# Performance work log

Hardware: AMD Instinct MI355X
Metric: run time of the kernel (lower is better)

Reference implementation:

```python
import jax, jax.numpy as jnp
import numpy as np

PHI = 1.618033988749895  # golden ratio
LUT_SIZE = 4096
TWO_PI = 2.0 * float(np.pi)
_grid = np.arange(LUT_SIZE, dtype=np.float32) * (TWO_PI / LUT_SIZE)
SIN_TABLE = jnp.asarray(np.sin(_grid).astype(np.float32))
COS_TABLE = jnp.asarray(np.cos(_grid).astype(np.float32))


def lut_sin_cos(theta):
    """4096-entry sin/cos lookup table over [0, 2pi) with linear interpolation."""
    pos = theta * (LUT_SIZE / TWO_PI)
    i0 = jnp.floor(pos)
    frac = (pos - i0).astype(theta.dtype)
    idx0 = jnp.mod(i0.astype(jnp.int32), LUT_SIZE)
    idx1 = jnp.mod(idx0 + 1, LUT_SIZE)
    sin_v = SIN_TABLE[idx0] * (1.0 - frac) + SIN_TABLE[idx1] * frac
    cos_v = COS_TABLE[idx0] * (1.0 - frac) + COS_TABLE[idx1] * frac
    return sin_v, cos_v


def _forward(input_ids, emb, w_query, b_query, w_key, b_key, w_ctx, W_res, B_res, w_pr, w_pi, w_out):
    B, S = input_ids.shape
    D = emb.shape[1] // 2
    H, dh = w_query.shape
    e = emb[input_ids]                               # [B,S,2D]
    w_emb, b_emb = e[..., :D], e[..., D:]
    t_arr = jnp.arange(S, dtype=jnp.float32)

    # --- sequential euler-transform recurrence (the only truly serial part) ---
    def step(carry, xs):
        h_r, h_i = carry
        w_t, b_t, t = xs                             # [B,D],[B,D],scalar
        wl = 1.0 + jnp.abs(w_t)
        tp = t * PHI
        th_r = h_r / wl + b_t + tp
        th_i = h_i / wl + b_t + tp
        sr, cr = lut_sin_cos(th_r)
        si, ci = lut_sin_cos(th_i)
        nr = cr * ci - sr * si
        ni = cr * si + sr * ci
        return (nr, ni), nr + ni

    init = (jnp.zeros((B, D), dtype=emb.dtype), jnp.zeros((B, D), dtype=emb.dtype))
    xs = (jnp.swapaxes(w_emb, 0, 1), jnp.swapaxes(b_emb, 0, 1), t_arr)
    _, states = jax.lax.scan(step, init, xs)         # [S,B,D]
    states = jnp.swapaxes(states, 0, 1)              # [B,S,D] == cached_states

    # --- multi-head LUT sin/cos attention over strictly-previous cached states ---
    xp = states.reshape(B, S, H, dh)                 # per-head patches
    t_phi = t_arr * PHI                              # [S]
    th_q = xp / (1.0 + jnp.abs(w_query)) + b_query + t_phi[None, :, None, None]
    sq, cq = lut_sin_cos(th_q)
    q = jnp.concatenate([cq, sq], axis=-1)           # [B,S,H,2dh]
    th_k = xp / (1.0 + jnp.abs(w_key)) + b_key
    sk, ck = lut_sin_cos(th_k)
    k = jnp.concatenate([ck, sk], axis=-1)           # [B,S,H,2dh]
    scale = float(np.sqrt(2.0 * dh))
    scores = jnp.einsum('bthd,bshd->bhts', q, k) / scale
    mask = jnp.tril(jnp.ones((S, S), dtype=bool), k=-1)   # keys strictly before query
    scores = jnp.where(mask[None, None], scores, -1e30)
    weights = jax.nn.softmax(scores, axis=-1)
    context = jnp.einsum('bhts,bsd->btd', weights, states)   # heads summed
    has_ctx = (t_arr > 0).astype(states.dtype)[None, :, None]  # t=0 has no cache
    x = states + has_ctx * (context @ w_ctx.T)

    # --- resonant layer over num_neurons ---
    wl_res = 1.0 + jnp.abs(W_res)                    # [N,D]
    theta = x[:, :, None, :] / wl_res + B_res + t_phi[None, :, None, None]  # [B,S,N,D]
    s_t, c_t = lut_sin_cos(theta)
    cos_sum = c_t.sum(-1)                            # [B,S,N]
    sin_sum = s_t.sum(-1)
    x = x + jax.nn.silu(cos_sum @ w_pr.T + sin_sum @ w_pi.T)

    return x @ w_out.T                               # [B,S,V]


def setup_inputs() -> dict:
    key = jax.random.key(0)
    ks = jax.random.split(key, 12)
    B, S, V, D, H, N = 8, 512, 32000, 64, 4, 128
    dh = D // H
    return {
        'input_ids': jax.random.randint(ks[0], (B, S), 0, V),
        'emb': jax.random.normal(ks[1], (V, 2 * D), dtype=jnp.float32) * 0.02,
        'w_query': jax.random.normal(ks[2], (H, dh), dtype=jnp.float32) * 0.02,
        'b_query': jnp.zeros((H, dh), dtype=jnp.float32),
        'w_key': jax.random.normal(ks[3], (H, dh), dtype=jnp.float32) * 0.02,
        'b_key': jnp.zeros((H, dh), dtype=jnp.float32),
        'w_ctx': jax.random.normal(ks[4], (D, D), dtype=jnp.float32) * 0.02,
        'W_res': jax.random.normal(ks[5], (N, D), dtype=jnp.float32) * 0.02,
        'B_res': jnp.zeros((N, D), dtype=jnp.float32),
        'w_pr': jax.random.normal(ks[6], (D, N), dtype=jnp.float32) * 0.02,
        'w_pi': jax.random.normal(ks[7], (D, N), dtype=jnp.float32) * 0.02,
        'w_out': jax.random.normal(ks[8], (V, D), dtype=jnp.float32) * 0.02,
    }


def reference(input_ids, emb, w_query, b_query, w_key, b_key, w_ctx, W_res, B_res, w_pr, w_pi, w_out):
    return _forward(input_ids, emb, w_query, b_query, w_key, b_key, w_ctx, W_res, B_res, w_pr, w_pi, w_out)
```

## Files before the change

### kernel.cpp

```cpp
#include <hip/hip_runtime.h>
#include <hip/hip_bf16.h>
#include <math.h>

#define PHI_F     1.618033988749895f
#define LUT_N     4096
#define LUT_INV   651.8986469044033f
#define LUT_STEP  0.0015339807878856412f

#define B_  8
#define S_  512
#define D_  64
#define H_  4
#define DH_ 16
#define N_  128
#define V_  32000
#define R_  (B_ * S_)

typedef __attribute__((ext_vector_type(8))) short short8_t;
typedef __attribute__((ext_vector_type(4))) float f32x4;

__device__ __forceinline__ void lut2(const float2* __restrict__ sc,
                                     float th, float& s, float& c) {
    float pos = th * LUT_INV;
    float f0  = floorf(pos);
    float fr  = pos - f0;
    int   i0  = ((int)f0) & (LUT_N - 1);
    int   i1  = (i0 + 1) & (LUT_N - 1);
    float2 p0 = sc[i0];
    float2 p1 = sc[i1];
    float om  = 1.0f - fr;
    s = p0.x * om + p1.x * fr;
    c = p0.y * om + p1.y * fr;
}

__global__ void k_tables(float2* __restrict__ scT) {
    int i = blockIdx.x * blockDim.x + threadIdx.x;
    if (i < LUT_N) {
        float g = (float)i * LUT_STEP;
        scT[i] = make_float2((float)sin((double)g), (float)cos((double)g));
    }
}

__global__ __launch_bounds__(256) void k_fused0(
        const int* __restrict__ ids, const float* __restrict__ emb,
        const float* __restrict__ Wres, const float* __restrict__ Bres,
        const float* __restrict__ wpr, const float* __restrict__ wpi,
        const float* __restrict__ wout, const float2* __restrict__ scT,
        float* __restrict__ states, __hip_bfloat16* __restrict__ wb,
        float2* __restrict__ ibres, float2* __restrict__ wpT) {
    int blk = blockIdx.x;
    int tid = threadIdx.x;
    if (blk >= 8) {
        if (blk < 2008) {
            int i = (blk - 8) * 256 + tid;
            float4 v = ((const float4*)wout)[i];
            union { __hip_bfloat16 h[4]; short4 s4; } u;
            u.h[0] = __float2bfloat16(v.x);
            u.h[1] = __float2bfloat16(v.y);
            u.h[2] = __float2bfloat16(v.z);
            u.h[3] = __float2bfloat16(v.w);
            *(short4*)(&wb[4 * (size_t)i]) = u.s4;
        } else {
            int idx = (blk - 2008) * 256 + tid;
            ibres[idx] = make_float2(1.0f / (1.0f + fabsf(Wres[idx])), Bres[idx]);
            int nn = idx >> 6, d = idx & 63;
            wpT[idx] = make_float2(wpr[d * N_ + nn], wpi[d * N_ + nn]);
        }
        return;
    }
    __shared__ float2 sc[LUT_N];
    __shared__ int idsh[S_];
    for (int i = tid; i < LUT_N; i += 256) sc[i] = scT[i];
    for (int i = tid; i < S_; i += 256) idsh[i] = ids[blk * S_ + i];
    __syncthreads();
    if (tid >= 64) return;
    int d = tid, b = blk;
    float cw[8], cb[8], nw[8], nb[8];
#pragma unroll
    for (int j = 0; j < 8; ++j) {
        int id = idsh[j];
        cw[j] = emb[(size_t)id * 128 + d];
        cb[j] = emb[(size_t)id * 128 + 64 + d];
    }
    float* outp = states + (size_t)b * S_ * D_ + d;
    float hr = 0.0f, hi = 0.0f;
    for (int tc = 0; tc < S_; tc += 8) {
#pragma unroll
        for (int jj = 0; jj < 8; ++jj) {
            int id = idsh[(tc + 8 + jj) & (S_ - 1)];
            nw[jj] = emb[(size_t)id * 128 + d];
            nb[jj] = emb[(size_t)id * 128 + 64 + d];
        }
#pragma unroll
        for (int jj = 0; jj < 8; ++jj) {
            int   t   = tc + jj;
            float wl  = 1.0f + fabsf(cw[jj]);
            float btv = cb[jj];
            float tp  = (float)t * PHI_F;
            float thr = hr / wl + btv + tp;
            float thi = hi / wl + btv + tp;
            float sr, cr, si, ci;
            lut2(sc, thr, sr, cr);
            lut2(sc, thi, si, ci);
            float nr = cr * ci - sr * si;
            float ni = cr * si + sr * ci;
            hr = nr; hi = ni;
            outp[t * D_] = nr + ni;
        }
#pragma unroll
        for (int jj = 0; jj < 8; ++jj) { cw[jj] = nw[jj]; cb[jj] = nb[jj]; }
    }
}

__global__ __launch_bounds__(256) void k_qk(const float* __restrict__ states,
                                            const float* __restrict__ wq,
                                            const float* __restrict__ bq,
                                            const float* __restrict__ wk,
                                            const float* __restrict__ bk,
                                            const float2* __restrict__ scT,
                                            float* __restrict__ q,
                                            float* __restrict__ kT) {
    __shared__ float2 sc[LUT_N];
    for (int i = threadIdx.x; i < LUT_N; i += 256) sc[i] = scT[i];
    __syncthreads();
    {
        int idx = blockIdx.x * 256 + threadIdx.x;
        int j  = idx & (DH_ - 1);
        int h  = (idx >> 4) & (H_ - 1);
        int bt = idx >> 6;
        int t  = bt & (S_ - 1);
        int b  = bt >> 9;
        float xp = states[idx];
        float tp = (float)t * PHI_F;
        int   hj = h * DH_ + j;
        float thq = xp / (1.0f + fabsf(wq[hj])) + bq[hj] + tp;
        float thk = xp / (1.0f + fabsf(wk[hj])) + bk[hj];
        float sq, cq, sk, ck;
        lut2(sc, thq, sq, cq);
        lut2(sc, thk, sk, ck);
        int base = bt * (H_ * 2 * DH_) + h * (2 * DH_) + j;
        q[base] = cq; q[base + DH_] = sq;
        size_t kb = ((size_t)(b * H_ + h) * 32 + j) * S_ + t;
        kT[kb] = ck; kT[kb + 16 * S_] = sk;
    }
}

#define TB_ 4
__global__ __launch_bounds__(256) void k_attn(const float* __restrict__ states,
                                              const float* __restrict__ q,
                                              const float* __restrict__ kT,
                                              const float* __restrict__ wctx,
                                              float* __restrict__ x) {
    __shared__ float ql[H_][TB_][2 * DH_];
    __shared__ float wlds[H_][TB_][S_];
    __shared__ float cpart[4][TB_][D_];
    __shared__ float ctx[TB_][D_];
    int blk = blockIdx.x;
    int b = blk >> 7, tile = blk & 127;
    int t0 = tile * TB_;
    int tid = threadIdx.x;
    int h = tid >> 6, l = tid & 63;
    if (l < 2 * DH_) {
#pragma unroll
        for (int tt = 0; tt < TB_; ++tt)
            ql[h][tt][l] = q[((b << 9) + t0 + tt) * 128 + h * 32 + l];
    }
    __syncthreads();

    const float* kTb = kT + (size_t)(b * H_ + h) * 32 * S_;
    float sc[8][TB_];
    float m[TB_];
#pragma unroll
    for (int tt = 0; tt < TB_; ++tt) m[tt] = -INFINITY;
#pragma unroll
    for (int jj = 0; jj < 8; ++jj) {
        int s = l + jj * 64;
        float a0 = 0.f, a1 = 0.f, a2 = 0.f, a3 = 0.f;
        if (s < t0 + TB_ - 1) {
#pragma unroll
            for (int c = 0; c < 32; ++c) {
                float kv = kTb[c * S_ + s];
                a0 = fmaf(kv, ql[h][0][c], a0);
                a1 = fmaf(kv, ql[h][1][c], a1);
                a2 = fmaf(kv, ql[h][2][c], a2);
                a3 = fmaf(kv, ql[h][3][c], a3);
            }
        }
        const float scale = 0.1767766952966369f;
        float v0 = (s < t0 + 0) ? a0 * scale : -INFINITY;
        float v1 = (s < t0 + 1) ? a1 * scale : -INFINITY;
        float v2 = (s < t0 + 2) ? a2 * scale : -INFINITY;
        float v3 = (s < t0 + 3) ? a3 * scale : -INFINITY;
        sc[jj][0] = v0; m[0] = fmaxf(m[0], v0);
        sc[jj][1] = v1; m[1] = fmaxf(m[1], v1);
        sc[jj][2] = v2; m[2] = fmaxf(m[2], v2);
        sc[jj][3] = v3; m[3] = fmaxf(m[3], v3);
    }
#pragma unroll
    for (int tt = 0; tt < TB_; ++tt)
        for (int o = 32; o; o >>= 1) m[tt] = fmaxf(m[tt], __shfl_xor(m[tt], o));
    float sum[TB_] = {0.f, 0.f, 0.f, 0.f};
#pragma unroll
    for (int jj = 0; jj < 8; ++jj)
#pragma unroll
        for (int tt = 0; tt < TB_; ++tt) {
            float e = __expf(sc[jj][tt] - m[tt]);
            sc[jj][tt] = e; sum[tt] += e;
        }
#pragma unroll
    for (int tt = 0; tt < TB_; ++tt)
        for (int o = 32; o; o >>= 1) sum[tt] += __shfl_xor(sum[tt], o);
#pragma unroll
    for (int tt = 0; tt < TB_; ++tt) {
        float inv = 1.0f / sum[tt];
#pragma unroll
        for (int jj = 0; jj < 8; ++jj)
            wlds[h][tt][l + jj * 64] = sc[jj][tt] * inv;
    }
    __syncthreads();
    {
        int p = tid >> 6, d = tid & 63;
        float ac[TB_] = {0.f, 0.f, 0.f, 0.f};
        for (int s = p; s < t0 + TB_ - 1; s += 4) {
            float sv = states[(((size_t)b << 9) + s) * D_ + d];
#pragma unroll
            for (int tt = 0; tt < TB_; ++tt) {
                float w4 = wlds[0][tt][s] + wlds[1][tt][s]
                         + wlds[2][tt][s] + wlds[3][tt][s];
                if (s < t0 + tt) ac[tt] += w4 * sv;
            }
        }
#pragma unroll
        for (int tt = 0; tt < TB_; ++tt) cpart[p][tt][d] = ac[tt];
    }
    __syncthreads();
    {
        int tt = tid >> 6, dd = tid & 63;
        ctx[tt][dd] = cpart[0][tt][dd] + cpart[1][tt][dd]
                    + cpart[2][tt][dd] + cpart[3][tt][dd];
    }
    __syncthreads();
    {
        int tt = tid >> 6, dd = tid & 63;
        int t  = t0 + tt;
        size_t row = ((size_t)b << 9) + t;
        float base = states[row * D_ + dd];
        float val  = base;
        if (t > 0) {
            float y = 0.0f;
            const float* wr = wctx + dd * D_;
            for (int k = 0; k < D_; ++k) y += ctx[tt][k] * wr[k];
            val = base + y;
        }
        x[row * D_ + dd] = val;
    }
}

__global__ __launch_bounds__(256) void k_resid(const float* __restrict__ x,
                                               const float2* __restrict__ ibres,
                                               const float2* __restrict__ wpT,
                                               const float2* __restrict__ scT,
                                               __hip_bfloat16* __restrict__ xb) {
    __shared__ float2 sc[LUT_N];
    __shared__ float xv[D_];
    __shared__ float csum[N_], ssum[N_];
    __shared__ float part[4][D_];
    int tid = threadIdx.x;
    for (int i = tid; i < LUT_N; i += 256) sc[i] = scT[i];
    int n  = tid >> 1;
    int d0 = (tid & 1) * 32;
    float2 ib[32];
#pragma unroll
    for (int dd = 0; dd < 32; ++dd) ib[dd] = ibres[n * D_ + d0 + dd];
    int g = tid >> 6, dl = tid & 63;
    for (int r = 0; r < 8; ++r) {
        int bt = blockIdx.x * 8 + r;
        int t  = bt & (S_ - 1);
        float tp = (float)t * PHI_F;
        __syncthreads();
        if (tid < D_) xv[tid] = x[bt * D_ + tid];
        __syncthreads();
        float cs = 0.0f, ss = 0.0f;
#pragma unroll
        for (int dd = 0; dd < 32; ++dd) {
            float th = fmaf(xv[d0 + dd], ib[dd].x, ib[dd].y) + tp;
            float s, c;
            lut2(sc, th, s, c);
            cs += c; ss += s;
        }
        cs += __shfl_xor(cs, 1);
        ss += __shfl_xor(ss, 1);
        if ((tid & 1) == 0) { csum[n] = cs; ssum[n] = ss; }
        __syncthreads();
        float acc = 0.0f;
#pragma unroll
        for (int nn = 0; nn < 32; ++nn) {
            float2 w = wpT[(g * 32 + nn) * D_ + dl];
            acc = fmaf(csum[g * 32 + nn], w.x, fmaf(ssum[g * 32 + nn], w.y, acc));
        }
        part[g][dl] = acc;
        __syncthreads();
        if (tid < D_) {
            float pre = part[0][tid] + part[1][tid] + part[2][tid] + part[3][tid];
            float sig = 1.0f / (1.0f + __expf(-pre));
            xb[bt * D_ + tid] = __float2bfloat16(xv[tid] + pre * sig);
        }
    }
}

__global__ __launch_bounds__(256) void k_out(const __hip_bfloat16* __restrict__ xb,
                                             const __hip_bfloat16* __restrict__ wb,
                                             float* __restrict__ out) {
    __shared__ float ot[64][132];
    int tid  = threadIdx.x;
    int wave = tid >> 6, l = tid & 63;
    int wr = wave >> 1, wc = wave & 1;
    int m0 = blockIdx.y * 64 + wr * 32;
    int r  = l & 15;
    int ks = (l >> 4) * 8;
    int kh = l >> 4;

    short8_t a[2][2];
#pragma unroll
    for (int mi = 0; mi < 2; ++mi)
#pragma unroll
        for (int kk = 0; kk < 2; ++kk)
            a[mi][kk] = *reinterpret_cast<const short8_t*>(
                xb + (size_t)(m0 + mi * 16 + r) * 64 + kk * 32 + ks);

    for (int ch = 0; ch < 2; ++ch) {
        int c0 = blockIdx.x * 256 + ch * 128 + wc * 64;
        short8_t b[4][2];
#pragma unroll
        for (int ni = 0; ni < 4; ++ni)
#pragma unroll
            for (int kk = 0; kk < 2; ++kk)
                b[ni][kk] = *reinterpret_cast<const short8_t*>(
                    wb + (size_t)(c0 + ni * 16 + r) * 64 + kk * 32 + ks);

        f32x4 acc[2][4];
#pragma unroll
        for (int mi = 0; mi < 2; ++mi)
#pragma unroll
            for (int ni = 0; ni < 4; ++ni) {
                acc[mi][ni] = (f32x4){0.f, 0.f, 0.f, 0.f};
                acc[mi][ni] = __builtin_amdgcn_mfma_f32_16x16x32_bf16(
                    a[mi][0], b[ni][0], acc[mi][ni], 0, 0, 0);
                acc[mi][ni] = __builtin_amdgcn_mfma_f32_16x16x32_bf16(
                    a[mi][1], b[ni][1], acc[mi][ni], 0, 0, 0);
            }

        if (ch) __syncthreads();
#pragma unroll
        for (int mi = 0; mi < 2; ++mi)
#pragma unroll
            for (int ni = 0; ni < 4; ++ni)
#pragma unroll
                for (int i = 0; i < 4; ++i)
                    ot[wr * 32 + mi * 16 + kh * 4 + i][wc * 64 + ni * 16 + r] = acc[mi][ni][i];
        __syncthreads();

        size_t rbase = blockIdx.y * 64;
        size_t cb    = (size_t)blockIdx.x * 256 + ch * 128;
#pragma unroll
        for (int j = 0; j < 8; ++j) {
            int idx = j * 256 + tid;
            int row = idx >> 5, c4 = idx & 31;
            f32x4 v = *(const f32x4*)&ot[row][c4 * 4];
            __builtin_nontemporal_store(v,
                (f32x4*)&out[(rbase + row) * V_ + cb + c4 * 4]);
        }
    }
}

extern "C" void kernel_launch(void* const* d_in, const int* in_sizes, int n_in,
                              void* d_out, int out_size, void* d_ws, size_t ws_size,
                              hipStream_t stream) {
    const int*   ids  = (const int*)  d_in[0];
    const float* emb  = (const float*)d_in[1];
    const float* wq   = (const float*)d_in[2];
    const float* bq   = (const float*)d_in[3];
    const float* wk   = (const float*)d_in[4];
    const float* bk   = (const float*)d_in[5];
    const float* wctx = (const float*)d_in[6];
    const float* Wres = (const float*)d_in[7];
    const float* Bres = (const float*)d_in[8];
    const float* wpr  = (const float*)d_in[9];
    const float* wpi  = (const float*)d_in[10];
    const float* wout = (const float*)d_in[11];
    float* out = (float*)d_out;

    float* states = (float*)d_ws;
    float* qbuf   = states + R_ * D_;
    float* kTbuf  = qbuf + R_ * 128;
    float* xbuf   = kTbuf + B_ * H_ * 32 * S_;
    __hip_bfloat16* wb = (__hip_bfloat16*)(xbuf + R_ * D_);
    __hip_bfloat16* xb = wb + (size_t)V_ * D_;
    float2* scT   = (float2*)(xb + R_ * D_);
    float2* ibres = scT + LUT_N;
    float2* wpT   = ibres + N_ * D_;

    k_tables<<<16, 256, 0, stream>>>(scT);
    k_fused0<<<2040, 256, 0, stream>>>(ids, emb, Wres, Bres, wpr, wpi, wout, scT,
                                       states, wb, ibres, wpT);
    k_qk    <<<1024, 256, 0, stream>>>(states, wq, bq, wk, bk, scT, qbuf, kTbuf);
    k_attn  <<<1024, 256, 0, stream>>>(states, qbuf, kTbuf, wctx, xbuf);
    k_resid <<<R_ / 8, 256, 0, stream>>>(xbuf, ibres, wpT, scT, xb);
    k_out   <<<dim3(V_ / 256, R_ / 64), 256, 0, stream>>>(xb, wb, out);
}
```

Before: 326.0 us.

## Use paired float4 LUT in recurrence, drop LDS tables in qk, batch resid loads

```diff
diff --git a/kernel.cpp b/kernel.cpp
--- a/kernel.cpp
+++ b/kernel.cpp
@@ -33,11 +33,15 @@
     c = p0.y * om + p1.y * fr;
 }
 
-__global__ void k_tables(float2* __restrict__ scT) {
+__global__ void k_tables(float2* __restrict__ scT2, float4* __restrict__ scT4) {
     int i = blockIdx.x * blockDim.x + threadIdx.x;
     if (i < LUT_N) {
         float g = (float)i * LUT_STEP;
-        scT[i] = make_float2((float)sin((double)g), (float)cos((double)g));
+        float s = (float)sin((double)g);
+        float c = (float)cos((double)g);
+        scT2[i] = make_float2(s, c);
+        *(float2*)&scT4[i] = make_float2(s, c);
+        *(((float2*)&scT4[(i - 1) & (LUT_N - 1)]) + 1) = make_float2(s, c);
     }
 }
 
@@ -45,7 +49,7 @@
         const int* __restrict__ ids, const float* __restrict__ emb,
         const float* __restrict__ Wres, const float* __restrict__ Bres,
         const float* __restrict__ wpr, const float* __restrict__ wpi,
-        const float* __restrict__ wout, const float2* __restrict__ scT,
+        const float* __restrict__ wout, const float4* __restrict__ scT4,
         float* __restrict__ states, __hip_bfloat16* __restrict__ wb,
         float2* __restrict__ ibres, float2* __restrict__ wpT) {
     int blk = blockIdx.x;
@@ -68,26 +72,26 @@
         }
         return;
     }
-    __shared__ float2 sc[LUT_N];
-    __shared__ int idsh[S_];
-    for (int i = tid; i < LUT_N; i += 256) sc[i] = scT[i];
-    for (int i = tid; i < S_; i += 256) idsh[i] = ids[blk * S_ + i];
+    __shared__ float4 sc4[LUT_N];
+    for (int i = tid; i < LUT_N; i += 256) sc4[i] = scT4[i];
     __syncthreads();
     if (tid >= 64) return;
     int d = tid, b = blk;
-    float cw[8], cb[8], nw[8], nb[8];
+    const int* idp = ids + b * S_;
+    float cw[8], cb[8];
 #pragma unroll
     for (int j = 0; j < 8; ++j) {
-        int id = idsh[j];
+        int id = idp[j];
         cw[j] = emb[(size_t)id * 128 + d];
         cb[j] = emb[(size_t)id * 128 + 64 + d];
     }
     float* outp = states + (size_t)b * S_ * D_ + d;
     float hr = 0.0f, hi = 0.0f;
     for (int tc = 0; tc < S_; tc += 8) {
+        float nw[8], nb[8], res[8];
 #pragma unroll
         for (int jj = 0; jj < 8; ++jj) {
-            int id = idsh[(tc + 8 + jj) & (S_ - 1)];
+            int id = idp[(tc + 8 + jj) & (S_ - 1)];
             nw[jj] = emb[(size_t)id * 128 + d];
             nb[jj] = emb[(size_t)id * 128 + 64 + d];
         }
@@ -99,14 +103,26 @@
             float tp  = (float)t * PHI_F;
             float thr = hr / wl + btv + tp;
             float thi = hi / wl + btv + tp;
-            float sr, cr, si, ci;
-            lut2(sc, thr, sr, cr);
-            lut2(sc, thi, si, ci);
+            float posr = thr * LUT_INV;
+            float posi = thi * LUT_INV;
+            float fr0 = floorf(posr), fi0 = floorf(posi);
+            float frr = posr - fr0,   fri = posi - fi0;
+            int   ir  = ((int)fr0) & (LUT_N - 1);
+            int   ii  = ((int)fi0) & (LUT_N - 1);
+            float4 pr = sc4[ir];
+            float4 pi = sc4[ii];
+            float omr = 1.0f - frr, omi = 1.0f - fri;
+            float sr = pr.x * omr + pr.z * frr;
+            float cr = pr.y * omr + pr.w * frr;
+            float si = pi.x * omi + pi.z * fri;
+            float ci = pi.y * omi + pi.w * fri;
             float nr = cr * ci - sr * si;
             float ni = cr * si + sr * ci;
             hr = nr; hi = ni;
-            outp[t * D_] = nr + ni;
-        }
+            res[jj] = nr + ni;
+        }
+#pragma unroll
+        for (int jj = 0; jj < 8; ++jj) outp[(tc + jj) * D_] = res[jj];
 #pragma unroll
         for (int jj = 0; jj < 8; ++jj) { cw[jj] = nw[jj]; cb[jj] = nb[jj]; }
     }
@@ -120,29 +136,24 @@
                                             const float2* __restrict__ scT,
                                             float* __restrict__ q,
                                             float* __restrict__ kT) {
-    __shared__ float2 sc[LUT_N];
-    for (int i = threadIdx.x; i < LUT_N; i += 256) sc[i] = scT[i];
-    __syncthreads();
-    {
-        int idx = blockIdx.x * 256 + threadIdx.x;
-        int j  = idx & (DH_ - 1);
-        int h  = (idx >> 4) & (H_ - 1);
-        int bt = idx >> 6;
-        int t  = bt & (S_ - 1);
-        int b  = bt >> 9;
-        float xp = states[idx];
-        float tp = (float)t * PHI_F;
-        int   hj = h * DH_ + j;
-        float thq = xp / (1.0f + fabsf(wq[hj])) + bq[hj] + tp;
-        float thk = xp / (1.0f + fabsf(wk[hj])) + bk[hj];
-        float sq, cq, sk, ck;
-        lut2(sc, thq, sq, cq);
-        lut2(sc, thk, sk, ck);
-        int base = bt * (H_ * 2 * DH_) + h * (2 * DH_) + j;
-        q[base] = cq; q[base + DH_] = sq;
-        size_t kb = ((size_t)(b * H_ + h) * 32 + j) * S_ + t;
-        kT[kb] = ck; kT[kb + 16 * S_] = sk;
-    }
+    int idx = blockIdx.x * 256 + threadIdx.x;
+    int j  = idx & (DH_ - 1);
+    int h  = (idx >> 4) & (H_ - 1);
+    int bt = idx >> 6;
+    int t  = bt & (S_ - 1);
+    int b  = bt >> 9;
+    float xp = states[idx];
+    float tp = (float)t * PHI_F;
+    int   hj = h * DH_ + j;
+    float thq = xp / (1.0f + fabsf(wq[hj])) + bq[hj] + tp;
+    float thk = xp / (1.0f + fabsf(wk[hj])) + bk[hj];
+    float sq, cq, sk, ck;
+    lut2(scT, thq, sq, cq);
+    lut2(scT, thk, sk, ck);
+    int base = bt * (H_ * 2 * DH_) + h * (2 * DH_) + j;
+    q[base] = cq; q[base + DH_] = sq;
+    size_t kb = ((size_t)(b * H_ + h) * 32 + j) * S_ + t;
+    kT[kb] = ck; kT[kb + 16 * S_] = sk;
 }
 
 #define TB_ 4
@@ -262,28 +273,32 @@
                                                const float2* __restrict__ scT,
                                                __hip_bfloat16* __restrict__ xb) {
     __shared__ float2 sc[LUT_N];
-    __shared__ float xv[D_];
+    __shared__ float xv8[8][D_];
     __shared__ float csum[N_], ssum[N_];
     __shared__ float part[4][D_];
     int tid = threadIdx.x;
     for (int i = tid; i < LUT_N; i += 256) sc[i] = scT[i];
+    {
+        int r2 = tid >> 5, o = tid & 31;
+        size_t base = (size_t)(blockIdx.x * 8 + r2) * D_;
+        xv8[r2][o]      = x[base + o];
+        xv8[r2][o + 32] = x[base + o + 32];
+    }
     int n  = tid >> 1;
     int d0 = (tid & 1) * 32;
     float2 ib[32];
 #pragma unroll
     for (int dd = 0; dd < 32; ++dd) ib[dd] = ibres[n * D_ + d0 + dd];
     int g = tid >> 6, dl = tid & 63;
+    __syncthreads();
     for (int r = 0; r < 8; ++r) {
         int bt = blockIdx.x * 8 + r;
         int t  = bt & (S_ - 1);
         float tp = (float)t * PHI_F;
-        __syncthreads();
-        if (tid < D_) xv[tid] = x[bt * D_ + tid];
-        __syncthreads();
         float cs = 0.0f, ss = 0.0f;
 #pragma unroll
         for (int dd = 0; dd < 32; ++dd) {
-            float th = fmaf(xv[d0 + dd], ib[dd].x, ib[dd].y) + tp;
+            float th = fmaf(xv8[r][d0 + dd], ib[dd].x, ib[dd].y) + tp;
             float s, c;
             lut2(sc, th, s, c);
             cs += c; ss += s;
@@ -303,7 +318,7 @@
         if (tid < D_) {
             float pre = part[0][tid] + part[1][tid] + part[2][tid] + part[3][tid];
             float sig = 1.0f / (1.0f + __expf(-pre));
-            xb[bt * D_ + tid] = __float2bfloat16(xv[tid] + pre * sig);
+            xb[bt * D_ + tid] = __float2bfloat16(xv8[r][tid] + pre * sig);
         }
     }
 }
@@ -399,9 +414,10 @@
     float2* scT   = (float2*)(xb + R_ * D_);
     float2* ibres = scT + LUT_N;
     float2* wpT   = ibres + N_ * D_;
-
-    k_tables<<<16, 256, 0, stream>>>(scT);
-    k_fused0<<<2040, 256, 0, stream>>>(ids, emb, Wres, Bres, wpr, wpi, wout, scT,
+    float4* scT4  = (float4*)(wpT + N_ * D_);
+
+    k_tables<<<16, 256, 0, stream>>>(scT, scT4);
+    k_fused0<<<2040, 256, 0, stream>>>(ids, emb, Wres, Bres, wpr, wpi, wout, scT4,
                                        states, wb, ibres, wpT);
     k_qk    <<<1024, 256, 0, stream>>>(states, wq, bq, wk, bk, scT, qbuf, kTbuf);
     k_attn  <<<1024, 256, 0, stream>>>(states, qbuf, kTbuf, wctx, xbuf);
```

Measured after the change: 321.3 us, median of 2. About the same (-1.4%).
